# Optimization experiments

Measured on AMD Instinct MI355X. Metric: run time of the kernel, lower is better.

The kernel has to match this reference:

```python
import jax, jax.numpy as jnp
import numpy as np

N, E, H, NH, RBF = 20000, 200000, 128, 8, 64
HD = H // NH
CUT_HI = 5.0


def _ln(t, s, b, eps=1e-6):
    mu = t.mean(-1, keepdims=True)
    var = ((t - mu) ** 2).mean(-1, keepdims=True)
    return (t - mu) * jax.lax.rsqrt(var + eps) * s + b


def _cutoff(w):
    # cosine cutoff, cutoff_lower = 0
    return 0.5 * (jnp.cos(w * (jnp.pi / CUT_HI)) + 1.0) * (w < CUT_HI)


def _xavier(k, fi, fo):
    lim = float(np.sqrt(6.0 / (fi + fo)))
    return jax.random.uniform(k, (fi, fo), minval=-lim, maxval=lim, dtype=jnp.float32)


def setup_inputs() -> dict:
    key = jax.random.key(0)
    ks = jax.random.split(key, 16)
    return {
        "x": jax.random.normal(ks[0], (N, H), jnp.float32),
        "vec": jax.random.normal(ks[1], (N, 3, H), jnp.float32),
        "edge_weight": jax.random.uniform(ks[2], (E, 1), jnp.float32) * 6.0,
        "edge_attr": jax.random.uniform(ks[3], (E, RBF), jnp.float32),
        "edge_vec": jax.random.normal(ks[4], (E, 3), jnp.float32),
        "senders": jax.random.randint(ks[5], (E,), 0, N, jnp.int32),
        "receivers": jax.random.randint(ks[6], (E,), 0, N, jnp.int32),
        "ln_s": jnp.ones((H,), jnp.float32), "ln_b": jnp.zeros((H,), jnp.float32),
        "Wq": _xavier(ks[7], H, H), "bq": jnp.zeros((H,), jnp.float32),
        "Wk": _xavier(ks[8], H, H), "bk": jnp.zeros((H,), jnp.float32),
        "Wv": _xavier(ks[9], H, 3 * H), "bv": jnp.zeros((3 * H,), jnp.float32),
        "Wvec": _xavier(ks[10], H, 3 * H),
        "Wdk": _xavier(ks[11], RBF, H), "bdk": jnp.zeros((H,), jnp.float32),
        "Wdv": _xavier(ks[12], RBF, 3 * H), "bdv": jnp.zeros((3 * H,), jnp.float32),
        "Wo": _xavier(ks[13], H, 3 * H), "bo": jnp.zeros((3 * H,), jnp.float32),
        "qln_s": jnp.ones((HD,), jnp.float32), "qln_b": jnp.zeros((HD,), jnp.float32),
        "kln_s": jnp.ones((HD,), jnp.float32), "kln_b": jnp.zeros((HD,), jnp.float32),
    }


def reference(x, vec, edge_weight, edge_attr, edge_vec, senders, receivers,
              ln_s, ln_b, Wq, bq, Wk, bk, Wv, bv, Wvec, Wdk, bdk, Wdv, bdv,
              Wo, bo, qln_s, qln_b, kln_s, kln_b):
    act = jax.nn.silu
    n = x.shape[0]
    xn = _ln(x, ln_s, ln_b)                                    # [N,H]
    q = _ln((xn @ Wq + bq).reshape(n, NH, HD), qln_s, qln_b)   # [N,h,d]
    k = _ln((xn @ Wk + bk).reshape(n, NH, HD), kln_s, kln_b)   # [N,h,d]
    v = (xn @ Wv + bv).reshape(n, NH, 3 * HD)                  # [N,h,3d]
    vp = vec @ Wvec                                            # [N,3,3H]
    vec1, vec2, vec3 = jnp.split(vp, 3, axis=-1)               # [N,3,H] each
    vec_dot = (vec1 * vec2).sum(axis=1)                        # [N,H]
    vec_h = vec.reshape(n, 3, NH, HD)                          # [N,3,h,d]
    dk = act(edge_attr @ Wdk + bdk).reshape(-1, NH, HD)        # [E,h,d]
    dv = act(edge_attr @ Wdv + bdv).reshape(-1, NH, 3 * HD)    # [E,h,3d]
    # message
    attn = (q[receivers] * k[senders] * dk).sum(axis=-1)       # [E,h]
    attn = act(attn) * _cutoff(edge_weight)                    # [E,h]
    v_j = v[senders] * dv                                      # [E,h,3d]
    xm, m1, m2 = jnp.split(v_j, 3, axis=2)                     # [E,h,d]
    xm = xm * attn[:, :, None]                                 # [E,h,d]
    vec_m = vec_h[senders] * m1[:, None] + m2[:, None] * edge_vec[:, :, None, None]  # [E,3,h,d]
    # aggregate
    x_agg = jax.ops.segment_sum(xm, receivers, num_segments=n).reshape(n, H)
    vec_agg = jax.ops.segment_sum(vec_m, receivers, num_segments=n).reshape(n, 3, H)
    o1, o2, o3 = jnp.split(x_agg @ Wo + bo, 3, axis=1)         # [N,H] each
    dvec = vec3 * o1[:, None] + vec_agg                        # [N,3,H]
    dx = vec_dot * o2 + o3                                     # [N,H]
    return (dx, dvec)
```

## Files before the change

### kernel.cpp

```cpp
#include <hip/hip_runtime.h>
#include <stdint.h>

#define NN 20000
#define NE 200000

typedef __attribute__((ext_vector_type(8))) short bf16x8;
typedef __attribute__((ext_vector_type(4))) float f32x4;

__device__ __forceinline__ float bf2f(uint32_t u) {
  union { uint32_t i; float f; } v; v.i = u << 16; return v.f;
}
__device__ __forceinline__ uint16_t f2bf(float f) {
  union { float f; uint32_t i; } v; v.f = f;
  return (uint16_t)((v.i + 0x7fffu + ((v.i >> 16) & 1u)) >> 16);
}
__device__ __forceinline__ uint32_t pk2(float lo, float hi) {
  return (uint32_t)f2bf(lo) | ((uint32_t)f2bf(hi) << 16);
}
__device__ __forceinline__ float siluf(float x) { return x / (1.f + __expf(-x)); }
__device__ __forceinline__ float prod2(uint32_t q2, uint32_t k2, uint32_t d2) {
  return bf2f(q2 & 0xffffu) * bf2f(k2 & 0xffffu) * bf2f(d2 & 0xffffu)
       + bf2f(q2 >> 16) * bf2f(k2 >> 16) * bf2f(d2 >> 16);
}

__global__ void k_prep(const float* __restrict__ Wq, const float* __restrict__ Wk,
                       const float* __restrict__ Wv, const float* __restrict__ Wvec,
                       const float* __restrict__ Wdk, const float* __restrict__ Wdv,
                       const float* __restrict__ Wo, const float* __restrict__ bq,
                       const float* __restrict__ bk, const float* __restrict__ bv,
                       const float* __restrict__ bdk, const float* __restrict__ bdv,
                       uint16_t* __restrict__ WTqkv, uint16_t* __restrict__ WTvec,
                       uint16_t* __restrict__ WTdkv2, uint16_t* __restrict__ WTo,
                       float* __restrict__ Bqkv, float* __restrict__ Bdkv2) {
  int idx = blockIdx.x * 256 + threadIdx.x;
  if (idx < 98304) {
    int rr = idx >> 7, k = idx & 127;
    float v;
    if (rr < 128)      v = Wq[k * 128 + rr];
    else if (rr < 256) v = Wk[k * 128 + rr - 128];
    else {
      int j2 = rr - 256, j = j2 >> 2, c = j2 & 3;
      v = (c < 3) ? Wv[k * 384 + (j >> 4) * 48 + c * 16 + (j & 15)] : 0.f;
    }
    WTqkv[idx] = f2bf(v);
    return;
  }
  idx -= 98304;
  if (idx < 49152) {
    int c = idx >> 7, k = idx & 127;
    WTvec[idx] = f2bf(Wvec[k * 384 + c]);
    return;
  }
  idx -= 49152;
  if (idx < 32768) {
    int rr = idx >> 6, k = idx & 63;
    float v;
    if (rr < 128) v = Wdk[k * 128 + rr];
    else {
      int j = rr - 128, p = j >> 7, hd = j & 127;
      v = Wdv[k * 384 + (hd >> 4) * 48 + p * 16 + (hd & 15)];
    }
    WTdkv2[idx] = f2bf(v);
    return;
  }
  idx -= 32768;
  if (idx < 49152) {
    int c = idx >> 7, k = idx & 127;
    WTo[idx] = f2bf(Wo[k * 384 + c]);
    return;
  }
  idx -= 49152;
  if (idx < 768) {
    if (idx < 128)      Bqkv[idx] = bq[idx];
    else if (idx < 256) Bqkv[idx] = bk[idx - 128];
    else {
      int j2 = idx - 256, j = j2 >> 2, c = j2 & 3;
      Bqkv[idx] = (c < 3) ? bv[(j >> 4) * 48 + c * 16 + (j & 15)] : 0.f;
    }
  } else if (idx < 1280) {
    int t = idx - 768;
    if (t < 128) Bdkv2[t] = bdk[t];
    else {
      int j = t - 128, p = j >> 7, hd = j & 127;
      Bdkv2[t] = bdv[(hd >> 4) * 48 + p * 16 + (hd & 15)];
    }
  }
}

__global__ void k_node_pre(const float* __restrict__ x, const float* __restrict__ s,
                           const float* __restrict__ b, const float* __restrict__ vec,
                           uint16_t* __restrict__ xn_b, uint16_t* __restrict__ combo) {
  if (blockIdx.x < 5000) {
    int gt = blockIdx.x * 256 + threadIdx.x;
    int node = gt >> 6, lane = gt & 63;
    if (node >= NN) return;
    const float* row = x + (size_t)node * 128;
    float2 v = *(const float2*)&row[lane * 2];
    float sum = v.x + v.y, sq = v.x * v.x + v.y * v.y;
    #pragma unroll
    for (int off = 32; off; off >>= 1) { sum += __shfl_xor(sum, off); sq += __shfl_xor(sq, off); }
    float mu = sum * (1.f / 128.f);
    float var = sq * (1.f / 128.f) - mu * mu;
    float rs = rsqrtf(var + 1e-6f);
    float o0 = (v.x - mu) * rs * s[lane * 2] + b[lane * 2];
    float o1 = (v.y - mu) * rs * s[lane * 2 + 1] + b[lane * 2 + 1];
    ((uint32_t*)xn_b)[(size_t)node * 64 + lane] = pk2(o0, o1);
  } else {
    int i = (blockIdx.x - 5000) * 256 + threadIdx.x;
    if (i >= NN * 128) return;
    int n = i >> 7, j = i & 127;
    const float* vr = vec + (size_t)n * 384 + j;
    uint2 o;
    o.x = pk2(vr[0], vr[128]);
    o.y = pk2(vr[256], 0.f);
    *(uint2*)&combo[(size_t)n * 1024 + j * 8 + 4] = o;
  }
}

__global__ void k_hist(const int* __restrict__ rcv, int* __restrict__ deg) {
  int e = blockIdx.x * 256 + threadIdx.x;
  if (e < NE) atomicAdd(&deg[rcv[e]], 1);
}

__global__ void k_scan1(const int* __restrict__ deg, int* __restrict__ bsum) {
  __shared__ int ws[4];
  int i = blockIdx.x * 256 + threadIdx.x;
  int x = (i < NN) ? deg[i] : 0;
  #pragma unroll
  for (int d = 32; d; d >>= 1) x += __shfl_xor(x, d);
  if ((threadIdx.x & 63) == 0) ws[threadIdx.x >> 6] = x;
  __syncthreads();
  if (threadIdx.x == 0) bsum[blockIdx.x] = ws[0] + ws[1] + ws[2] + ws[3];
}

__global__ void k_scan2(int* __restrict__ bsum, int nb, int* __restrict__ off) {
  int lane = threadIdx.x;
  int carry = 0;
  for (int base = 0; base < nb; base += 64) {
    int i = base + lane;
    int x = (i < nb) ? bsum[i] : 0;
    int v = x;
    #pragma unroll
    for (int d = 1; d < 64; d <<= 1) { int y = __shfl_up(v, d); if (lane >= d) v += y; }
    if (i < nb) bsum[i] = carry + v - x;
    carry += __shfl(v, 63);
  }
  if (lane == 0) off[NN] = carry;
}

__global__ void k_scan3(const int* __restrict__ deg, const int* __restrict__ bsum,
                        int* __restrict__ off, int* __restrict__ cur) {
  __shared__ int ws[4];
  int t = threadIdx.x, lane = t & 63, w = t >> 6;
  int i = blockIdx.x * 256 + t;
  int x = (i < NN) ? deg[i] : 0;
  int v = x;
  #pragma unroll
  for (int d = 1; d < 64; d <<= 1) { int y = __shfl_up(v, d); if (lane >= d) v += y; }
  if (lane == 63) ws[w] = v;
  __syncthreads();
  int wadd = 0;
  for (int j = 0; j < w; j++) wadd += ws[j];
  int excl = bsum[blockIdx.x] + wadd + v - x;
  if (i < NN) { off[i] = excl; cur[i] = excl; }
}

__global__ void k_scatter(const int* __restrict__ rcv, int* __restrict__ cur,
                          int* __restrict__ perm) {
  int e = blockIdx.x * 256 + threadIdx.x;
  if (e >= NE) return;
  int pos = atomicAdd(&cur[rcv[e]], 1);
  perm[pos] = e;
}

__global__ void k_permute(const float* __restrict__ ea, const int* __restrict__ perm,
                          const int* __restrict__ snd, const int* __restrict__ rcv,
                          const float* __restrict__ ew, const float* __restrict__ evec,
                          uint16_t* __restrict__ ea_perm, int* __restrict__ sndp,
                          int* __restrict__ rcvp, float4* __restrict__ edata) {
  int idx = blockIdx.x * 256 + threadIdx.x;
  if (idx >= NE * 16) return;
  int i = idx >> 4, j = idx & 15;
  int e = perm[i];
  float4 v = *(const float4*)&ea[(size_t)e * 64 + j * 4];
  uint2 o;
  o.x = pk2(v.x, v.y);
  o.y = pk2(v.z, v.w);
  *(uint2*)&ea_perm[(size_t)i * 64 + j * 4] = o;
  if (j == 0) {
    sndp[i] = snd[e];
    rcvp[i] = rcv[e];
    float w = ew[e];
    float cut = (w < 5.f) ? 0.5f * (__cosf(w * 0.628318530717958648f) + 1.f) : 0.f;
    edata[i] = make_float4(evec[e * 3], evec[e * 3 + 1], evec[e * 3 + 2], cut);
  }
}

template <int KTOT, bool OUT_BF16, bool SILU, bool AF32>
__global__ __launch_bounds__(256) void k_gemm(const void* __restrict__ A,
                                              const uint16_t* __restrict__ BT,
                                              const float* __restrict__ bias,
                                              void* __restrict__ Cout, int M, int Fo) {
  __shared__ __align__(16) uint16_t As[128 * 72];
  __shared__ __align__(16) uint16_t Bs[128 * 72];
  const uint16_t* A16 = (const uint16_t*)A;
  const float* A32 = (const float*)A;
  int t = threadIdx.x;
  int l = t & 63;
  int row0 = blockIdx.y * 128, col0 = blockIdx.x * 128;
  int wm = ((t >> 6) >> 1) * 64, wn = ((t >> 6) & 1) * 64;
  f32x4 acc[4][4] = {};
  for (int kt = 0; kt < KTOT; kt += 64) {
    __syncthreads();
    #pragma unroll
    for (int i = 0; i < 4; i++) {
      int c = i * 256 + t;
      int row = c >> 3, ko = (c & 7) * 8;
      uint4 av = make_uint4(0u, 0u, 0u, 0u);
      int gr = row0 + row;
      if (gr < M) {
        if (AF32) {
          float4 f0 = *(const float4*)&A32[(size_t)gr * KTOT + kt + ko];
          float4 f1 = *(const float4*)&A32[(size_t)gr * KTOT + kt + ko + 4];
          av = make_uint4(pk2(f0.x, f0.y), pk2(f0.z, f0.w), pk2(f1.x, f1.y), pk2(f1.z, f1.w));
        } else {
          av = *(const uint4*)&A16[(size_t)gr * KTOT + kt + ko];
        }
      }
      *(uint4*)&As[row * 72 + ko] = av;
      uint4 bw = *(const uint4*)&BT[(size_t)(col0 + row) * KTOT + kt + ko];
      *(uint4*)&Bs[row * 72 + ko] = bw;
    }
    __syncthreads();
    #pragma unroll
    for (int kk = 0; kk < 64; kk += 32) {
      bf16x8 af[4], bfr[4];
      #pragma unroll
      for (int mf = 0; mf < 4; mf++)
        af[mf] = *(const bf16x8*)&As[(wm + mf * 16 + (l & 15)) * 72 + (l >> 4) * 8 + kk];
      #pragma unroll
      for (int nf = 0; nf < 4; nf++)
        bfr[nf] = *(const bf16x8*)&Bs[(wn + nf * 16 + (l & 15)) * 72 + (l >> 4) * 8 + kk];
      #pragma unroll
      for (int mf = 0; mf < 4; mf++)
        #pragma unroll
        for (int nf = 0; nf < 4; nf++)
          acc[mf][nf] = __builtin_amdgcn_mfma_f32_16x16x32_bf16(af[mf], bfr[nf], acc[mf][nf], 0, 0, 0);
    }
  }
  float* Cf = (float*)Cout;
  uint16_t* Cb = (uint16_t*)Cout;
  #pragma unroll
  for (int mf = 0; mf < 4; mf++) {
    #pragma unroll
    for (int r = 0; r < 4; r++) {
      int grow = row0 + wm + mf * 16 + (l >> 4) * 4 + r;
      if (grow >= M) continue;
      #pragma unroll
      for (int nf = 0; nf < 4; nf++) {
        int gcol = col0 + wn + nf * 16 + (l & 15);
        float v = acc[mf][nf][r];
        if (bias) v += bias[gcol];
        if (SILU) v = siluf(v);
        if (OUT_BF16) Cb[(size_t)grow * Fo + gcol] = f2bf(v);
        else          Cf[(size_t)grow * Fo + gcol] = v;
      }
    }
  }
}

__global__ __launch_bounds__(256) void k_gemm_qkv(
    const uint16_t* __restrict__ A, const uint16_t* __restrict__ BT,
    const float* __restrict__ bias, const float* __restrict__ qs,
    const float* __restrict__ qb, const float* __restrict__ ks,
    const float* __restrict__ kb, uint16_t* __restrict__ qk_b,
    uint16_t* __restrict__ combo) {
  __shared__ __align__(16) uint16_t As[128 * 72];
  __shared__ __align__(16) uint16_t Bs[128 * 72];
  int t = threadIdx.x;
  int l = t & 63;
  int row0 = blockIdx.y * 128, col0 = blockIdx.x * 128;
  int wm = ((t >> 6) >> 1) * 64, wn = ((t >> 6) & 1) * 64;
  f32x4 acc[4][4] = {};
  for (int kt = 0; kt < 128; kt += 64) {
    __syncthreads();
    #pragma unroll
    for (int i = 0; i < 4; i++) {
      int c = i * 256 + t;
      int row = c >> 3, ko = (c & 7) * 8;
      uint4 av = make_uint4(0u, 0u, 0u, 0u);
      int gr = row0 + row;
      if (gr < NN) av = *(const uint4*)&A[(size_t)gr * 128 + kt + ko];
      *(uint4*)&As[row * 72 + ko] = av;
      uint4 bw = *(const uint4*)&BT[(size_t)(col0 + row) * 128 + kt + ko];
      *(uint4*)&Bs[row * 72 + ko] = bw;
    }
    __syncthreads();
    #pragma unroll
    for (int kk = 0; kk < 64; kk += 32) {
      bf16x8 af[4], bfr[4];
      #pragma unroll
      for (int mf = 0; mf < 4; mf++)
        af[mf] = *(const bf16x8*)&As[(wm + mf * 16 + (l & 15)) * 72 + (l >> 4) * 8 + kk];
      #pragma unroll
      for (int nf = 0; nf < 4; nf++)
        bfr[nf] = *(const bf16x8*)&Bs[(wn + nf * 16 + (l & 15)) * 72 + (l >> 4) * 8 + kk];
      #pragma unroll
      for (int mf = 0; mf < 4; mf++)
        #pragma unroll
        for (int nf = 0; nf < 4; nf++)
          acc[mf][nf] = __builtin_amdgcn_mfma_f32_16x16x32_bf16(af[mf], bfr[nf], acc[mf][nf], 0, 0, 0);
    }
  }
  int d = l & 15;
  if (col0 < 256) {
    float sc_q = qs[d], bb_q = qb[d], sc_k = ks[d], bb_k = kb[d];
    #pragma unroll
    for (int mf = 0; mf < 4; mf++) {
      #pragma unroll
      for (int r = 0; r < 4; r++) {
        int grow = row0 + wm + mf * 16 + (l >> 4) * 4 + r;
        bool ok = grow < NN;
        #pragma unroll
        for (int nf = 0; nf < 4; nf++) {
          int gcol = col0 + wn + nf * 16 + d;
          float v = acc[mf][nf][r] + bias[gcol];
          float s1 = v;
          s1 += __shfl_xor(s1, 1); s1 += __shfl_xor(s1, 2);
          s1 += __shfl_xor(s1, 4); s1 += __shfl_xor(s1, 8);
          float mu = s1 * (1.f / 16.f);
          float dd = v - mu;
          float s2 = dd * dd;
          s2 += __shfl_xor(s2, 1); s2 += __shfl_xor(s2, 2);
          s2 += __shfl_xor(s2, 4); s2 += __shfl_xor(s2, 8);
          float rs = rsqrtf(s2 * (1.f / 16.f) + 1e-6f);
          bool isq = gcol < 128;
          float ov = dd * rs * (isq ? sc_q : sc_k) + (isq ? bb_q : bb_k);
          if (ok) qk_b[(size_t)grow * 256 + gcol] = f2bf(ov);
        }
      }
    }
  } else {
    #pragma unroll
    for (int mf = 0; mf < 4; mf++) {
      #pragma unroll
      for (int r = 0; r < 4; r++) {
        int grow = row0 + wm + mf * 16 + (l >> 4) * 4 + r;
        if (grow >= NN) continue;
        #pragma unroll
        for (int nf = 0; nf < 4; nf++) {
          int gcol = col0 + wn + nf * 16 + d;
          int j2 = gcol - 256, j = j2 >> 2, c = j2 & 3;
          if (c < 3)
            combo[(size_t)grow * 1024 + j * 8 + c] = f2bf(acc[mf][nf][r] + bias[gcol]);
        }
      }
    }
  }
}

#define MTS 516

__device__ __forceinline__ void mfma32(const uint16_t* As, int r0,
                                       const uint16_t* __restrict__ BT2, int cb,
                                       int wn, int l, f32x4 acc[2][2]) {
  #pragma unroll
  for (int kk = 0; kk < 2; kk++) {
    bf16x8 af[2];
    #pragma unroll
    for (int mf = 0; mf < 2; mf++)
      af[mf] = *(const bf16x8*)&As[(r0 + mf * 16 + (l & 15)) * 68 + (l >> 4) * 8 + kk * 32];
    #pragma unroll
    for (int nf = 0; nf < 2; nf++) {
      bf16x8 bv = *(const bf16x8*)&BT2[(size_t)(cb * 128 + wn + nf * 16 + (l & 15)) * 64 +
                                       (l >> 4) * 8 + kk * 32];
      #pragma unroll
      for (int mf = 0; mf < 2; mf++)
        acc[mf][nf] = __builtin_amdgcn_mfma_f32_16x16x32_bf16(af[mf], bv, acc[mf][nf], 0, 0, 0);
    }
  }
}

__device__ __forceinline__ void silu_slot(uint16_t* mt, const float bsv[2], int slot,
                                          int wn, int l, f32x4 acc[2][2]) {
  #pragma unroll
  for (int mf = 0; mf < 2; mf++)
    #pragma unroll
    for (int r = 0; r < 4; r++) {
      int row = mf * 16 + (l >> 4) * 4 + r;
      #pragma unroll
      for (int nf = 0; nf < 2; nf++) {
        int c = wn + nf * 16 + (l & 15);
        mt[row * MTS + c * 4 + slot] = f2bf(siluf(acc[mf][nf][r] + bsv[nf]));
      }
    }
}

__device__ __forceinline__ void silu_dk(uint16_t* mtd, const float bsv[2],
                                        int wn, int l, f32x4 acc[2][2]) {
  #pragma unroll
  for (int mf = 0; mf < 2; mf++)
    #pragma unroll
    for (int r = 0; r < 4; r++) {
      int row = mf * 16 + (l >> 4) * 4 + r;
      #pragma unroll
      for (int nf = 0; nf < 2; nf++) {
        int c = wn + nf * 16 + (l & 15);
        mtd[row * 140 + c] = f2bf(siluf(acc[mf][nf][r] + bsv[nf]));
      }
    }
}

__global__ __launch_bounds__(256) void k_edge_all(
    const uint16_t* __restrict__ eap, const int* __restrict__ sndp,
    const int* __restrict__ rcvp, const int* __restrict__ off,
    const float4* __restrict__ edata, const uint16_t* __restrict__ WT2,
    const float* __restrict__ Bd2, const uint16_t* __restrict__ qk_b,
    const uint16_t* __restrict__ combo, float* __restrict__ xagg,
    float* __restrict__ vecagg) {
  __shared__ __align__(16) uint16_t As[64 * 68];
  __shared__ __align__(16) uint16_t mt[32 * MTS];
  __shared__ __align__(16) uint16_t mtd[32 * 140];
  __shared__ float attn_l[32 * 8];
  __shared__ int sndl[64], rcvl[64], lo_g[64], hi_g[64];
  __shared__ float4 ed4[64];

  int e0 = blockIdx.x * 64;
  int t = threadIdx.x, l = t & 63, wn = (t >> 6) * 32;

  if (t < 64) {
    int e = e0 + t;
    int r = rcvp[e];
    sndl[t] = sndp[e]; rcvl[t] = r;
    lo_g[t] = off[r]; hi_g[t] = off[r + 1];
    ed4[t] = edata[e];
  }
  #pragma unroll
  for (int i = 0; i < 2; i++) {
    int c = i * 256 + t;
    int row = c >> 3, ko = (c & 7) * 8;
    *(uint4*)&As[row * 68 + ko] = *(const uint4*)&eap[(size_t)(e0 + row) * 64 + ko];
  }
  float bs[4][2];
  #pragma unroll
  for (int cb = 0; cb < 4; cb++) {
    bs[cb][0] = Bd2[cb * 128 + wn + (l & 15)];
    bs[cb][1] = Bd2[cb * 128 + wn + 16 + (l & 15)];
  }
  __syncthreads();

  #pragma unroll
  for (int half = 0; half < 2; half++) {
    int r0 = half * 32;
    { f32x4 acc[2][2] = {}; mfma32(As, r0, WT2, 0, wn, l, acc); silu_dk(mtd, bs[0], wn, l, acc); }
    __syncthreads();
    {
      int el = t >> 3, h = t & 7;
      int ge = r0 + el;
      int rn = rcvl[ge], sn = sndl[ge];
      const uint16_t* qb_ = qk_b + (size_t)rn * 256 + h * 16;
      const uint16_t* kb_ = qk_b + (size_t)sn * 256 + 128 + h * 16;
      uint4 q0 = *(const uint4*)qb_;
      uint4 q1 = *(const uint4*)(qb_ + 8);
      uint4 k0 = *(const uint4*)kb_;
      uint4 k1 = *(const uint4*)(kb_ + 8);
      { f32x4 acc[2][2] = {}; mfma32(As, r0, WT2, 1, wn, l, acc); silu_slot(mt, bs[1], 0, wn, l, acc); }
      { f32x4 acc[2][2] = {}; mfma32(As, r0, WT2, 2, wn, l, acc); silu_slot(mt, bs[2], 1, wn, l, acc); }
      { f32x4 acc[2][2] = {}; mfma32(As, r0, WT2, 3, wn, l, acc); silu_slot(mt, bs[3], 2, wn, l, acc); }
      const uint32_t* dp = (const uint32_t*)&mtd[el * 140 + h * 16];
      uint32_t qa[8] = {q0.x, q0.y, q0.z, q0.w, q1.x, q1.y, q1.z, q1.w};
      uint32_t ka[8] = {k0.x, k0.y, k0.z, k0.w, k1.x, k1.y, k1.z, k1.w};
      float dot = 0.f;
      #pragma unroll
      for (int j = 0; j < 8; j++) dot += prod2(qa[j], ka[j], dp[j]);
      attn_l[el * 8 + h] = siluf(dot) * ed4[ge].w;
    }
    __syncthreads();
    {
      int col = t & 127, sub = t >> 7;
      int i0 = r0 + sub * 16, i1 = i0 + 16;
      int ha = col >> 4;
      float accx = 0.f, a0 = 0.f, a1 = 0.f, a2 = 0.f;
      #pragma unroll 8
      for (int i = i0; i < i1; i++) {
        int li = i - r0;
        int n = rcvl[i], s = sndl[i];
        uint4 cv = *(const uint4*)&combo[(size_t)s * 1024 + col * 8];
        uint2 mr = *(const uint2*)&mt[li * MTS + col * 4];
        float a = attn_l[li * 8 + ha];
        float xmv = bf2f(mr.x & 0xffffu), m1v = bf2f(mr.x >> 16), m2v = bf2f(mr.y & 0xffffu);
        accx += bf2f(cv.x & 0xffffu) * xmv * a;
        float mm1 = bf2f(cv.x >> 16) * m1v;
        float mm2 = bf2f(cv.y & 0xffffu) * m2v;
        float4 ev = ed4[i];
        a0 += bf2f(cv.z & 0xffffu) * mm1 + ev.x * mm2;
        a1 += bf2f(cv.z >> 16)     * mm1 + ev.y * mm2;
        a2 += bf2f(cv.w & 0xffffu) * mm1 + ev.z * mm2;
        if (i == i1 - 1 || rcvl[i + 1] != n) {
          bool cont = (lo_g[i] >= e0 + i0) && (hi_g[i] <= e0 + i1);
          float* dx_ = &xagg[(size_t)n * 128 + col];
          float* d0 = &vecagg[((size_t)n * 3 + 0) * 128 + col];
          float* d1 = &vecagg[((size_t)n * 3 + 1) * 128 + col];
          float* d2 = &vecagg[((size_t)n * 3 + 2) * 128 + col];
          if (cont) { *dx_ = accx; *d0 = a0; *d1 = a1; *d2 = a2; }
          else { atomicAdd(dx_, accx); atomicAdd(d0, a0); atomicAdd(d1, a1); atomicAdd(d2, a2); }
          accx = a0 = a1 = a2 = 0.f;
        }
      }
    }
    __syncthreads();
  }
}

__global__ void k_final(const float* __restrict__ o, const uint16_t* __restrict__ vp,
                        float* __restrict__ dx, float* __restrict__ dvec) {
  int idx = blockIdx.x * 256 + threadIdx.x;
  if (idx >= NN * 128) return;
  int n = idx >> 7, j = idx & 127;
  const float* op = o + (size_t)n * 384;
  float o1 = op[j], o2 = op[128 + j], o3 = op[256 + j];
  const uint16_t* vpn = vp + (size_t)n * 3 * 384;
  float vd = 0.f;
  #pragma unroll
  for (int c = 0; c < 3; c++)
    vd += bf2f(vpn[c * 384 + j]) * bf2f(vpn[c * 384 + 128 + j]);
  dx[idx] = vd * o2 + o3;
  #pragma unroll
  for (int c = 0; c < 3; c++) {
    size_t vi = ((size_t)n * 3 + c) * 128 + j;
    dvec[vi] = bf2f(vpn[c * 384 + 256 + j]) * o1 + dvec[vi];
  }
}

static inline int cdiv_i(long long a, long long b) { return (int)((a + b - 1) / b); }

extern "C" void kernel_launch(void* const* d_in, const int* in_sizes, int n_in,
                              void* d_out, int out_size, void* d_ws, size_t ws_size,
                              hipStream_t stream) {
  const float* x    = (const float*)d_in[0];
  const float* vec  = (const float*)d_in[1];
  const float* ew   = (const float*)d_in[2];
  const float* ea   = (const float*)d_in[3];
  const float* evec = (const float*)d_in[4];
  const int*   snd  = (const int*)d_in[5];
  const int*   rcv  = (const int*)d_in[6];
  const float* ln_s = (const float*)d_in[7];
  const float* ln_b = (const float*)d_in[8];
  const float* Wq = (const float*)d_in[9];   const float* bq = (const float*)d_in[10];
  const float* Wk = (const float*)d_in[11];  const float* bk = (const float*)d_in[12];
  const float* Wv = (const float*)d_in[13];  const float* bv = (const float*)d_in[14];
  const float* Wvec = (const float*)d_in[15];
  const float* Wdk = (const float*)d_in[16]; const float* bdk = (const float*)d_in[17];
  const float* Wdv = (const float*)d_in[18]; const float* bdv = (const float*)d_in[19];
  const float* Wo = (const float*)d_in[20];  const float* bo = (const float*)d_in[21];
  const float* qln_s = (const float*)d_in[22]; const float* qln_b = (const float*)d_in[23];
  const float* kln_s = (const float*)d_in[24]; const float* kln_b = (const float*)d_in[25];
  (void)in_sizes; (void)n_in; (void)ws_size;

  uint8_t* p = (uint8_t*)d_ws;
  auto alloc = [&](size_t bytes) -> uint8_t* {
    uint8_t* r = p; p += (bytes + 255) & ~(size_t)255; return r;
  };
  uint16_t* WTqkv = (uint16_t*)alloc(768 * 128 * 2);
  float*    Bqkv  = (float*)alloc(768 * 4);
  uint16_t* WTvec = (uint16_t*)alloc(384 * 128 * 2);
  uint16_t* WTdkv = (uint16_t*)alloc(512 * 64 * 2);
  float*    Bdkv  = (float*)alloc(512 * 4);
  uint16_t* WTo   = (uint16_t*)alloc(384 * 128 * 2);
  int*      deg   = (int*)alloc(NN * 4);
  int*      off   = (int*)alloc((NN + 1) * 4);
  int*      cur   = (int*)alloc(NN * 4);
  int*      bsum  = (int*)alloc(256 * 4);
  int*      perm  = (int*)alloc((size_t)NE * 4);
  int*      sndp  = (int*)alloc((size_t)NE * 4);
  int*      rcvp  = (int*)alloc((size_t)NE * 4);
  float4*   edata = (float4*)alloc((size_t)NE * 16);
  uint16_t* ea_perm = (uint16_t*)alloc((size_t)NE * 64 * 2);
  uint16_t* xn_b  = (uint16_t*)alloc((size_t)NN * 128 * 2);
  uint16_t* combo = (uint16_t*)alloc((size_t)NN * 1024 * 2);
  uint16_t* qk_b  = (uint16_t*)alloc((size_t)NN * 256 * 2);
  uint16_t* vp    = (uint16_t*)alloc((size_t)NN * 3 * 384 * 2);
  float*    o     = (float*)alloc((size_t)NN * 384 * 4);

  float* xagg   = (float*)d_out;
  float* vecagg = (float*)d_out + (size_t)NN * 128;

  hipMemsetAsync(d_out, 0, (size_t)out_size * 4, stream);

  k_prep<<<cdiv_i(98304 + 49152 + 32768 + 49152 + 1280, 256), 256, 0, stream>>>(
      Wq, Wk, Wv, Wvec, Wdk, Wdv, Wo, bq, bk, bv, bdk, bdv,
      WTqkv, WTvec, WTdkv, WTo, Bqkv, Bdkv);

  int NSB = cdiv_i(NN, 256);
  hipMemsetAsync(deg, 0, NN * 4, stream);
  k_hist<<<cdiv_i(NE, 256), 256, 0, stream>>>(rcv, deg);
  k_scan1<<<NSB, 256, 0, stream>>>(deg, bsum);
  k_scan2<<<1, 64, 0, stream>>>(bsum, NSB, off);
  k_scan3<<<NSB, 256, 0, stream>>>(deg, bsum, off, cur);
  k_scatter<<<cdiv_i(NE, 256), 256, 0, stream>>>(rcv, cur, perm);
  k_permute<<<cdiv_i((long long)NE * 16, 256), 256, 0, stream>>>(ea, perm, snd, rcv, ew, evec,
                                                                 ea_perm, sndp, rcvp, edata);

  k_node_pre<<<5000 + cdiv_i((long long)NN * 128, 256), 256, 0, stream>>>(
      x, ln_s, ln_b, vec, xn_b, combo);

  { dim3 g(6, cdiv_i(NN, 128));
    k_gemm_qkv<<<g, 256, 0, stream>>>(xn_b, WTqkv, Bqkv, qln_s, qln_b, kln_s, kln_b,
                                      qk_b, combo); }

  { dim3 g(384 / 128, cdiv_i((long long)NN * 3, 128));
    k_gemm<128, true, false, true><<<g, 256, 0, stream>>>(vec, WTvec, nullptr, vp, NN * 3, 384); }

  k_edge_all<<<NE / 64, 256, 0, stream>>>(ea_perm, sndp, rcvp, off, edata, WTdkv, Bdkv,
                                          qk_b, combo, xagg, vecagg);

  { dim3 g(384 / 128, cdiv_i(NN, 128));
    k_gemm<128, false, false, true><<<g, 256, 0, stream>>>(xagg, WTo, bo, o, NN, 384); }

  k_final<<<cdiv_i((long long)NN * 128, 256), 256, 0, stream>>>(o, vp, xagg, vecagg);
}
```

Measured before the change: 354.4 us.

## Fuse output GEMM with final combine and pack combo rows to six bf16 per channel

Replaces the separate output-projection GEMM and elementwise final kernel with one kernel. Each block computes all three 128-column slices of x_agg@Wo in registers, then applies the vec_dot/vec3 combine directly, so the fp32 intermediate o no longer goes through global memory. Separately, the per-node combo buffer is compacted from 8 to 6 bf16 per channel, cutting gather bytes in the edge kernel at the cost of unaligned 32-bit loads. The fused kernel holds three accumulator sets and launches fewer blocks, which may reduce occupancy and parallelism.

```diff
diff --git a/kernel.cpp b/kernel.cpp
--- a/kernel.cpp
+++ b/kernel.cpp
@@ -110,10 +110,9 @@
     if (i >= NN * 128) return;
     int n = i >> 7, j = i & 127;
     const float* vr = vec + (size_t)n * 384 + j;
-    uint2 o;
-    o.x = pk2(vr[0], vr[128]);
-    o.y = pk2(vr[256], 0.f);
-    *(uint2*)&combo[(size_t)n * 1024 + j * 8 + 4] = o;
+    uint16_t* cb = &combo[(size_t)n * 768 + j * 6];
+    cb[3] = f2bf(vr[0]);
+    *(uint32_t*)&cb[4] = pk2(vr[128], vr[256]);
   }
 }
 
@@ -352,7 +351,91 @@
           int gcol = col0 + wn + nf * 16 + d;
           int j2 = gcol - 256, j = j2 >> 2, c = j2 & 3;
           if (c < 3)
-            combo[(size_t)grow * 1024 + j * 8 + c] = f2bf(acc[mf][nf][r] + bias[gcol]);
+            combo[(size_t)grow * 768 + j * 6 + c] = f2bf(acc[mf][nf][r] + bias[gcol]);
+        }
+      }
+    }
+  }
+}
+
+__device__ __forceinline__ void o_pass(const float* __restrict__ A32,
+                                       const uint16_t* __restrict__ BT, int row0, int cb,
+                                       int t, int l, int wm, int wn,
+                                       uint16_t* As, uint16_t* Bs, f32x4 (&acc)[4][4]) {
+  for (int kt = 0; kt < 128; kt += 64) {
+    __syncthreads();
+    #pragma unroll
+    for (int i = 0; i < 4; i++) {
+      int c = i * 256 + t;
+      int row = c >> 3, ko = (c & 7) * 8;
+      uint4 av = make_uint4(0u, 0u, 0u, 0u);
+      int gr = row0 + row;
+      if (gr < NN) {
+        float4 f0 = *(const float4*)&A32[(size_t)gr * 128 + kt + ko];
+        float4 f1 = *(const float4*)&A32[(size_t)gr * 128 + kt + ko + 4];
+        av = make_uint4(pk2(f0.x, f0.y), pk2(f0.z, f0.w), pk2(f1.x, f1.y), pk2(f1.z, f1.w));
+      }
+      *(uint4*)&As[row * 72 + ko] = av;
+      uint4 bw = *(const uint4*)&BT[(size_t)(cb * 128 + row) * 128 + kt + ko];
+      *(uint4*)&Bs[row * 72 + ko] = bw;
+    }
+    __syncthreads();
+    #pragma unroll
+    for (int kk = 0; kk < 64; kk += 32) {
+      bf16x8 af[4], bfr[4];
+      #pragma unroll
+      for (int mf = 0; mf < 4; mf++)
+        af[mf] = *(const bf16x8*)&As[(wm + mf * 16 + (l & 15)) * 72 + (l >> 4) * 8 + kk];
+      #pragma unroll
+      for (int nf = 0; nf < 4; nf++)
+        bfr[nf] = *(const bf16x8*)&Bs[(wn + nf * 16 + (l & 15)) * 72 + (l >> 4) * 8 + kk];
+      #pragma unroll
+      for (int mf = 0; mf < 4; mf++)
+        #pragma unroll
+        for (int nf = 0; nf < 4; nf++)
+          acc[mf][nf] = __builtin_amdgcn_mfma_f32_16x16x32_bf16(af[mf], bfr[nf], acc[mf][nf], 0, 0, 0);
+    }
+  }
+}
+
+__global__ __launch_bounds__(256) void k_gemm_o(
+    const uint16_t* __restrict__ BT, const float* __restrict__ bo,
+    const uint16_t* __restrict__ vp, float* __restrict__ dout) {
+  __shared__ __align__(16) uint16_t As[128 * 72];
+  __shared__ __align__(16) uint16_t Bs[128 * 72];
+  float* xagg = dout;
+  float* vecagg = dout + (size_t)NN * 128;
+  int t = threadIdx.x;
+  int l = t & 63;
+  int row0 = blockIdx.y * 128;
+  int wm = ((t >> 6) >> 1) * 64, wn = ((t >> 6) & 1) * 64;
+  f32x4 acc0[4][4] = {}, acc1[4][4] = {}, acc2[4][4] = {};
+  o_pass(xagg, BT, row0, 0, t, l, wm, wn, As, Bs, acc0);
+  o_pass(xagg, BT, row0, 1, t, l, wm, wn, As, Bs, acc1);
+  o_pass(xagg, BT, row0, 2, t, l, wm, wn, As, Bs, acc2);
+  int d = l & 15;
+  #pragma unroll
+  for (int mf = 0; mf < 4; mf++) {
+    #pragma unroll
+    for (int r = 0; r < 4; r++) {
+      int grow = row0 + wm + mf * 16 + (l >> 4) * 4 + r;
+      if (grow >= NN) continue;
+      const uint16_t* vpn = vp + (size_t)grow * 1152;
+      #pragma unroll
+      for (int nf = 0; nf < 4; nf++) {
+        int col = wn + nf * 16 + d;
+        float o1 = acc0[mf][nf][r] + bo[col];
+        float o2 = acc1[mf][nf][r] + bo[128 + col];
+        float o3 = acc2[mf][nf][r] + bo[256 + col];
+        float vd = 0.f;
+        #pragma unroll
+        for (int c = 0; c < 3; c++)
+          vd += bf2f(vpn[c * 384 + col]) * bf2f(vpn[c * 384 + 128 + col]);
+        xagg[(size_t)grow * 128 + col] = vd * o2 + o3;
+        #pragma unroll
+        for (int c = 0; c < 3; c++) {
+          size_t vi = ((size_t)grow * 3 + c) * 128 + col;
+          vecagg[vi] = bf2f(vpn[c * 384 + 256 + col]) * o1 + vecagg[vi];
         }
       }
     }
@@ -485,17 +568,20 @@
       for (int i = i0; i < i1; i++) {
         int li = i - r0;
         int n = rcvl[i], s = sndl[i];
-        uint4 cv = *(const uint4*)&combo[(size_t)s * 1024 + col * 8];
+        const uint16_t* cp = &combo[(size_t)s * 768 + col * 6];
+        uint32_t u0 = *(const uint32_t*)cp;
+        uint32_t u1 = *(const uint32_t*)(cp + 2);
+        uint32_t u2 = *(const uint32_t*)(cp + 4);
         uint2 mr = *(const uint2*)&mt[li * MTS + col * 4];
         float a = attn_l[li * 8 + ha];
         float xmv = bf2f(mr.x & 0xffffu), m1v = bf2f(mr.x >> 16), m2v = bf2f(mr.y & 0xffffu);
-        accx += bf2f(cv.x & 0xffffu) * xmv * a;
-        float mm1 = bf2f(cv.x >> 16) * m1v;
-        float mm2 = bf2f(cv.y & 0xffffu) * m2v;
+        accx += bf2f(u0 & 0xffffu) * xmv * a;
+        float mm1 = bf2f(u0 >> 16) * m1v;
+        float mm2 = bf2f(u1 & 0xffffu) * m2v;
         float4 ev = ed4[i];
-        a0 += bf2f(cv.z & 0xffffu) * mm1 + ev.x * mm2;
-        a1 += bf2f(cv.z >> 16)     * mm1 + ev.y * mm2;
-        a2 += bf2f(cv.w & 0xffffu) * mm1 + ev.z * mm2;
+        a0 += bf2f(u1 >> 16)     * mm1 + ev.x * mm2;
+        a1 += bf2f(u2 & 0xffffu) * mm1 + ev.y * mm2;
+        a2 += bf2f(u2 >> 16)     * mm1 + ev.z * mm2;
         if (i == i1 - 1 || rcvl[i + 1] != n) {
           bool cont = (lo_g[i] >= e0 + i0) && (hi_g[i] <= e0 + i1);
           float* dx_ = &xagg[(size_t)n * 128 + col];
@@ -509,26 +595,6 @@
       }
     }
     __syncthreads();
-  }
-}
-
-__global__ void k_final(const float* __restrict__ o, const uint16_t* __restrict__ vp,
-                        float* __restrict__ dx, float* __restrict__ dvec) {
-  int idx = blockIdx.x * 256 + threadIdx.x;
-  if (idx >= NN * 128) return;
-  int n = idx >> 7, j = idx & 127;
-  const float* op = o + (size_t)n * 384;
-  float o1 = op[j], o2 = op[128 + j], o3 = op[256 + j];
-  const uint16_t* vpn = vp + (size_t)n * 3 * 384;
-  float vd = 0.f;
-  #pragma unroll
-  for (int c = 0; c < 3; c++)
-    vd += bf2f(vpn[c * 384 + j]) * bf2f(vpn[c * 384 + 128 + j]);
-  dx[idx] = vd * o2 + o3;
-  #pragma unroll
-  for (int c = 0; c < 3; c++) {
-    size_t vi = ((size_t)n * 3 + c) * 128 + j;
-    dvec[vi] = bf2f(vpn[c * 384 + 256 + j]) * o1 + dvec[vi];
   }
 }
 
@@ -577,10 +643,9 @@
   float4*   edata = (float4*)alloc((size_t)NE * 16);
   uint16_t* ea_perm = (uint16_t*)alloc((size_t)NE * 64 * 2);
   uint16_t* xn_b  = (uint16_t*)alloc((size_t)NN * 128 * 2);
-  uint16_t* combo = (uint16_t*)alloc((size_t)NN * 1024 * 2);
+  uint16_t* combo = (uint16_t*)alloc((size_t)NN * 768 * 2);
   uint16_t* qk_b  = (uint16_t*)alloc((size_t)NN * 256 * 2);
   uint16_t* vp    = (uint16_t*)alloc((size_t)NN * 3 * 384 * 2);
-  float*    o     = (float*)alloc((size_t)NN * 384 * 4);
 
   float* xagg   = (float*)d_out;
   float* vecagg = (float*)d_out + (size_t)NN * 128;
@@ -614,8 +679,6 @@
   k_edge_all<<<NE / 64, 256, 0, stream>>>(ea_perm, sndp, rcvp, off, edata, WTdkv, Bdkv,
                                           qk_b, combo, xagg, vecagg);
 
-  { dim3 g(384 / 128, cdiv_i(NN, 128));
-    k_gemm<128, false, false, true><<<g, 256, 0, stream>>>(xagg, WTo, bo, o, NN, 384); }
-
-  k_final<<<cdiv_i((long long)NN * 128, 256), 256, 0, stream>>>(o, vp, xagg, vecagg);
-}
+  { dim3 g(1, cdiv_i(NN, 128));
+    k_gemm_o<<<g, 256, 0, stream>>>(WTo, bo, vp, (float*)d_out); }
+}
```

After: 356.2 us. No clear change (+0.5%).

## Pack combo node buffer to 6 bf16 per column and split head layernorm

Applied to the files above, without the earlier changes.

Shrinks the per-node combo record from 8 to 6 bf16 values per channel, dropping the padding slots. This cuts the bytes gathered per edge in the edge kernel, now read as three 32-bit loads instead of one 16-byte load. The per-head q/k layernorm moves out of the QKV GEMM epilogue, where it used shuffle reductions, into a separate k_headln kernel working on a raw bf16 buffer. That adds a kernel launch, an extra round trip of q/k through memory, and an extra bf16 rounding of q/k before the normalisation.

```diff
diff --git a/kernel.cpp b/kernel.cpp
--- a/kernel.cpp
+++ b/kernel.cpp
@@ -110,10 +110,9 @@
     if (i >= NN * 128) return;
     int n = i >> 7, j = i & 127;
     const float* vr = vec + (size_t)n * 384 + j;
-    uint2 o;
-    o.x = pk2(vr[0], vr[128]);
-    o.y = pk2(vr[256], 0.f);
-    *(uint2*)&combo[(size_t)n * 1024 + j * 8 + 4] = o;
+    uint16_t* cb = &combo[(size_t)n * 768 + j * 6];
+    cb[3] = f2bf(vr[0]);
+    *(uint32_t*)&cb[4] = pk2(vr[128], vr[256]);
   }
 }
 
@@ -269,11 +268,9 @@
   }
 }
 
-__global__ __launch_bounds__(256) void k_gemm_qkv(
+__global__ __launch_bounds__(256) void k_gemm_qkv2(
     const uint16_t* __restrict__ A, const uint16_t* __restrict__ BT,
-    const float* __restrict__ bias, const float* __restrict__ qs,
-    const float* __restrict__ qb, const float* __restrict__ ks,
-    const float* __restrict__ kb, uint16_t* __restrict__ qk_b,
+    const float* __restrict__ bias, uint16_t* __restrict__ qk_raw,
     uint16_t* __restrict__ combo) {
   __shared__ __align__(16) uint16_t As[128 * 72];
   __shared__ __align__(16) uint16_t Bs[128 * 72];
@@ -313,50 +310,46 @@
     }
   }
   int d = l & 15;
-  if (col0 < 256) {
-    float sc_q = qs[d], bb_q = qb[d], sc_k = ks[d], bb_k = kb[d];
-    #pragma unroll
-    for (int mf = 0; mf < 4; mf++) {
-      #pragma unroll
-      for (int r = 0; r < 4; r++) {
-        int grow = row0 + wm + mf * 16 + (l >> 4) * 4 + r;
-        bool ok = grow < NN;
-        #pragma unroll
-        for (int nf = 0; nf < 4; nf++) {
-          int gcol = col0 + wn + nf * 16 + d;
-          float v = acc[mf][nf][r] + bias[gcol];
-          float s1 = v;
-          s1 += __shfl_xor(s1, 1); s1 += __shfl_xor(s1, 2);
-          s1 += __shfl_xor(s1, 4); s1 += __shfl_xor(s1, 8);
-          float mu = s1 * (1.f / 16.f);
-          float dd = v - mu;
-          float s2 = dd * dd;
-          s2 += __shfl_xor(s2, 1); s2 += __shfl_xor(s2, 2);
-          s2 += __shfl_xor(s2, 4); s2 += __shfl_xor(s2, 8);
-          float rs = rsqrtf(s2 * (1.f / 16.f) + 1e-6f);
-          bool isq = gcol < 128;
-          float ov = dd * rs * (isq ? sc_q : sc_k) + (isq ? bb_q : bb_k);
-          if (ok) qk_b[(size_t)grow * 256 + gcol] = f2bf(ov);
+  #pragma unroll
+  for (int mf = 0; mf < 4; mf++) {
+    #pragma unroll
+    for (int r = 0; r < 4; r++) {
+      int grow = row0 + wm + mf * 16 + (l >> 4) * 4 + r;
+      if (grow >= NN) continue;
+      #pragma unroll
+      for (int nf = 0; nf < 4; nf++) {
+        int gcol = col0 + wn + nf * 16 + d;
+        float v = acc[mf][nf][r] + bias[gcol];
+        if (col0 < 256) {
+          qk_raw[(size_t)grow * 256 + gcol] = f2bf(v);
+        } else {
+          int j2 = gcol - 256, j = j2 >> 2, c = j2 & 3;
+          if (c < 3) combo[(size_t)grow * 768 + j * 6 + c] = f2bf(v);
         }
       }
     }
-  } else {
-    #pragma unroll
-    for (int mf = 0; mf < 4; mf++) {
-      #pragma unroll
-      for (int r = 0; r < 4; r++) {
-        int grow = row0 + wm + mf * 16 + (l >> 4) * 4 + r;
-        if (grow >= NN) continue;
-        #pragma unroll
-        for (int nf = 0; nf < 4; nf++) {
-          int gcol = col0 + wn + nf * 16 + d;
-          int j2 = gcol - 256, j = j2 >> 2, c = j2 & 3;
-          if (c < 3)
-            combo[(size_t)grow * 1024 + j * 8 + c] = f2bf(acc[mf][nf][r] + bias[gcol]);
-        }
-      }
-    }
-  }
+  }
+}
+
+__global__ void k_headln(const uint16_t* __restrict__ qkv, const float* __restrict__ qs,
+                         const float* __restrict__ qb, const float* __restrict__ ks,
+                         const float* __restrict__ kb, uint16_t* __restrict__ out) {
+  int idx = blockIdx.x * 256 + threadIdx.x;
+  if (idx >= NN * 16) return;
+  int n = idx >> 4, ph = idx & 15, part = ph >> 3, h = ph & 7;
+  const uint16_t* src = qkv + (size_t)n * 256 + part * 128 + h * 16;
+  float v[16], sum = 0.f;
+  #pragma unroll
+  for (int i = 0; i < 16; i++) { v[i] = bf2f(src[i]); sum += v[i]; }
+  float mu = sum * (1.f / 16.f), var = 0.f;
+  #pragma unroll
+  for (int i = 0; i < 16; i++) { float dd = v[i] - mu; var += dd * dd; }
+  float rs = rsqrtf(var * (1.f / 16.f) + 1e-6f);
+  const float* sc = part ? ks : qs;
+  const float* bb = part ? kb : qb;
+  uint16_t* dst = out + (size_t)n * 256 + part * 128 + h * 16;
+  #pragma unroll
+  for (int i = 0; i < 16; i++) dst[i] = f2bf((v[i] - mu) * rs * sc[i] + bb[i]);
 }
 
 #define MTS 516
@@ -485,17 +478,20 @@
       for (int i = i0; i < i1; i++) {
         int li = i - r0;
         int n = rcvl[i], s = sndl[i];
-        uint4 cv = *(const uint4*)&combo[(size_t)s * 1024 + col * 8];
+        const uint16_t* cp = &combo[(size_t)s * 768 + col * 6];
+        uint32_t u0 = *(const uint32_t*)cp;
+        uint32_t u1 = *(const uint32_t*)(cp + 2);
+        uint32_t u2 = *(const uint32_t*)(cp + 4);
         uint2 mr = *(const uint2*)&mt[li * MTS + col * 4];
         float a = attn_l[li * 8 + ha];
         float xmv = bf2f(mr.x & 0xffffu), m1v = bf2f(mr.x >> 16), m2v = bf2f(mr.y & 0xffffu);
-        accx += bf2f(cv.x & 0xffffu) * xmv * a;
-        float mm1 = bf2f(cv.x >> 16) * m1v;
-        float mm2 = bf2f(cv.y & 0xffffu) * m2v;
+        accx += bf2f(u0 & 0xffffu) * xmv * a;
+        float mm1 = bf2f(u0 >> 16) * m1v;
+        float mm2 = bf2f(u1 & 0xffffu) * m2v;
         float4 ev = ed4[i];
-        a0 += bf2f(cv.z & 0xffffu) * mm1 + ev.x * mm2;
-        a1 += bf2f(cv.z >> 16)     * mm1 + ev.y * mm2;
-        a2 += bf2f(cv.w & 0xffffu) * mm1 + ev.z * mm2;
+        a0 += bf2f(u1 >> 16)     * mm1 + ev.x * mm2;
+        a1 += bf2f(u2 & 0xffffu) * mm1 + ev.y * mm2;
+        a2 += bf2f(u2 >> 16)     * mm1 + ev.z * mm2;
         if (i == i1 - 1 || rcvl[i + 1] != n) {
           bool cont = (lo_g[i] >= e0 + i0) && (hi_g[i] <= e0 + i1);
           float* dx_ = &xagg[(size_t)n * 128 + col];
@@ -577,8 +573,9 @@
   float4*   edata = (float4*)alloc((size_t)NE * 16);
   uint16_t* ea_perm = (uint16_t*)alloc((size_t)NE * 64 * 2);
   uint16_t* xn_b  = (uint16_t*)alloc((size_t)NN * 128 * 2);
-  uint16_t* combo = (uint16_t*)alloc((size_t)NN * 1024 * 2);
+  uint16_t* qk_raw = (uint16_t*)alloc((size_t)NN * 256 * 2);
   uint16_t* qk_b  = (uint16_t*)alloc((size_t)NN * 256 * 2);
+  uint16_t* combo = (uint16_t*)alloc((size_t)NN * 768 * 2);
   uint16_t* vp    = (uint16_t*)alloc((size_t)NN * 3 * 384 * 2);
   float*    o     = (float*)alloc((size_t)NN * 384 * 4);
 
@@ -605,8 +602,9 @@
       x, ln_s, ln_b, vec, xn_b, combo);
 
   { dim3 g(6, cdiv_i(NN, 128));
-    k_gemm_qkv<<<g, 256, 0, stream>>>(xn_b, WTqkv, Bqkv, qln_s, qln_b, kln_s, kln_b,
-                                      qk_b, combo); }
+    k_gemm_qkv2<<<g, 256, 0, stream>>>(xn_b, WTqkv, Bqkv, qk_raw, combo); }
+  k_headln<<<cdiv_i((long long)NN * 16, 256), 256, 0, stream>>>(qk_raw, qln_s, qln_b,
+                                                               kln_s, kln_b, qk_b);
 
   { dim3 g(384 / 128, cdiv_i((long long)NN * 3, 128));
     k_gemm<128, true, false, true><<<g, 256, 0, stream>>>(vec, WTvec, nullptr, vp, NN * 3, 384); }
```

Result: faster. 342.6 us (-3.3%).
